# Optimization experiments

Hardware: AMD Instinct MI355X
Metric: run time of the kernel (lower is better)

The kernel has to match this reference:

```python
import jax, jax.numpy as jnp
import numpy as np

NUM_HEADS = 32
ROPE_BASE = 10000.0
MASK_NEG = -66504.0  # from (1 - tril) * -66504.0 in the source


def _rotate_half(x):
    d = x.shape[-1] // 2
    return jnp.concatenate([-x[..., d:], x[..., :d]], axis=-1)


def setup_inputs() -> dict:
    key = jax.random.key(0)
    k1, k2, k3, k4 = jax.random.split(key, 4)
    S, B, E = 2048, 2, 2048
    return {
        "hidden_states": jax.random.normal(k1, (S, B, E), dtype=jnp.float32) * 0.02,
        "qkv_w": jax.random.normal(k2, (E, 3 * E), dtype=jnp.float32) * 0.02,
        "qkv_b": jax.random.normal(k3, (3 * E,), dtype=jnp.float32) * 0.02,
        "out_w": jax.random.normal(k4, (E, E), dtype=jnp.float32) * 0.02,
        "out_b": jnp.zeros((E,), dtype=jnp.float32),
    }


def reference(hidden_states, qkv_w, qkv_b, out_w, out_b):
    # seq-first prompt/prefill path of IPEXTransformerAtten
    S, B, E = hidden_states.shape
    H = NUM_HEADS
    D = E // H

    # fused QKV projection (mm_qkv_out)
    qkv = jnp.einsum('sbe,ef->sbf', hidden_states, qkv_w) + qkv_b  # [S,B,3E]
    q, k, v = jnp.split(qkv, 3, axis=-1)
    q = q.reshape(S, B, H, D)
    k = k.reshape(S, B, H, D)
    v = v.reshape(S, B, H, D)

    # rotary embedding (GPT-NeoX style, full head_dim)
    inv_freq = 1.0 / (ROPE_BASE ** (jnp.arange(0, D, 2, dtype=jnp.float32) / D))
    freqs = jnp.arange(S, dtype=jnp.float32)[:, None] * inv_freq  # [S, D/2]
    emb = jnp.concatenate([freqs, freqs], axis=-1)  # [S, D]
    cos = jnp.cos(emb)[:, None, None, :].astype(hidden_states.dtype)
    sin = jnp.sin(emb)[:, None, None, :].astype(hidden_states.dtype)
    q = q * cos + _rotate_half(q) * sin
    k = k * cos + _rotate_half(k) * sin

    # scaled dot-product attention with causal mask
    scale = 1.0 / jnp.sqrt(jnp.array(D, dtype=hidden_states.dtype))
    scores = jnp.einsum('sbhd,tbhd->bhst', q, k) * scale  # [B,H,S,S]
    causal = jnp.tril(jnp.ones((S, S), dtype=scores.dtype))
    scores = scores + (1.0 - causal) * MASK_NEG
    attn = jax.nn.softmax(scores, axis=-1)
    ctx = jnp.einsum('bhst,tbhd->sbhd', attn, v).reshape(S, B, E)

    # output projection
    return jnp.einsum('sbe,ef->sbf', ctx, out_w) + out_b
```

## Files before the change

### kernel.cpp

```cpp
#include <hip/hip_runtime.h>
#include <hip/hip_bf16.h>

#define S_LEN 2048
#define BATCH 2
#define EMB   2048
#define NH    32
#define HD    64
#define M_ROWS (S_LEN * BATCH)
#define QKV_N  (3 * EMB)

typedef short bf16x8 __attribute__((ext_vector_type(8)));
typedef float f32x4  __attribute__((ext_vector_type(4)));

__device__ __forceinline__ unsigned short f2bf(float f) {
  unsigned int u = __float_as_uint(f);
  u += 0x7fffu + ((u >> 16) & 1u);
  return (unsigned short)(u >> 16);
}
__device__ __forceinline__ float bf2f(unsigned short h) {
  return __uint_as_float(((unsigned int)h) << 16);
}
__device__ __forceinline__ void async_copy16(const void* g, void* lds) {
  __builtin_amdgcn_global_load_lds(
      (const __attribute__((address_space(1))) void*)g,
      (__attribute__((address_space(3))) void*)lds, 16, 0, 0);
}

#if __has_builtin(__builtin_amdgcn_exp2f)
#define EXP2F(x) __builtin_amdgcn_exp2f(x)
#else
#define EXP2F(x) __expf((x) * 0.6931471805599453f)
#endif


__global__ __launch_bounds__(256) void cast_to_bf16(
    const float* __restrict__ in, unsigned short* __restrict__ out, int n4) {
  int i = blockIdx.x * 256 + threadIdx.x;
  if (i >= n4) return;
  float4 v = reinterpret_cast<const float4*>(in)[i];
  ushort4 o;
  o.x = f2bf(v.x); o.y = f2bf(v.y); o.z = f2bf(v.z); o.w = f2bf(v.w);
  reinterpret_cast<ushort4*>(out)[i] = o;
}

__global__ __launch_bounds__(256) void transpose_cast(
    const float* __restrict__ in, unsigned short* __restrict__ out, int R, int C) {
  __shared__ float tile[32][33];
  const int bc = blockIdx.x * 32, br = blockIdx.y * 32;
  const int tx = threadIdx.x & 31, ty = threadIdx.x >> 5;
  #pragma unroll
  for (int rr = ty; rr < 32; rr += 8)
    tile[rr][tx] = in[(size_t)(br + rr) * C + bc + tx];
  __syncthreads();
  #pragma unroll
  for (int rr = ty; rr < 32; rr += 8)
    out[(size_t)(bc + rr) * R + br + tx] = f2bf(tile[tx][rr]);
}


__global__ __launch_bounds__(256) void gemm_qkv(
    const unsigned short* __restrict__ A,
    const unsigned short* __restrict__ Wt,
    const float* __restrict__ bias,
    unsigned short* __restrict__ Qo,
    unsigned short* __restrict__ Ko,
    unsigned short* __restrict__ Vo) {
  __shared__ __align__(16) unsigned short As[128 * 32];
  __shared__ __align__(16) unsigned short Bs[128 * 32];
  const int tid = threadIdx.x;
  const int n0 = blockIdx.x * 128;
  const int m0 = blockIdx.y * 128;
  const int wave = tid >> 6, lane = tid & 63;
  const int wm = (wave >> 1) * 64, wn = (wave & 1) * 64;
  const int lm = lane & 15, lq = lane >> 4;
  const int K = 2048;

  const int r0 = tid >> 2, kc0 = (tid & 3) * 8;
  const unsigned short* Ar0 = A  + (size_t)(m0 + r0) * K + kc0;
  const unsigned short* Ar1 = Ar0 + (size_t)64 * K;
  const unsigned short* Br0 = Wt + (size_t)(n0 + r0) * K + kc0;
  const unsigned short* Br1 = Br0 + (size_t)64 * K;
  unsigned short* As0 = As + tid * 8;
  unsigned short* As1 = As + (tid + 256) * 8;
  unsigned short* Bs0 = Bs + tid * 8;
  unsigned short* Bs1 = Bs + (tid + 256) * 8;

  f32x4 acc[4][4] = {};

  for (int k0 = 0; k0 < K; k0 += 32) {
    async_copy16(Ar0 + k0, As0);
    async_copy16(Ar1 + k0, As1);
    async_copy16(Br0 + k0, Bs0);
    async_copy16(Br1 + k0, Bs1);
    __syncthreads();
    bf16x8 a[4], b[4];
    #pragma unroll
    for (int i = 0; i < 4; i++)
      a[i] = *reinterpret_cast<const bf16x8*>(As + (wm + i*16 + lm) * 32 + lq*8);
    #pragma unroll
    for (int j = 0; j < 4; j++)
      b[j] = *reinterpret_cast<const bf16x8*>(Bs + (wn + j*16 + lm) * 32 + lq*8);
    #pragma unroll
    for (int i = 0; i < 4; i++)
      #pragma unroll
      for (int j = 0; j < 4; j++)
        acc[i][j] = __builtin_amdgcn_mfma_f32_16x16x32_bf16(a[i], b[j], acc[i][j], 0, 0, 0);
    __syncthreads();
  }

  const int which = n0 >> 11;
  unsigned short* dst = (which == 0) ? Qo : (which == 1) ? Ko : Vo;
  #pragma unroll
  for (int j = 0; j < 4; j++) {
    const int n = n0 + wn + j*16 + lm;
    const float bv = bias[n];
    const int e = n & (EMB - 1), h = e >> 6, d = e & 63;
    #pragma unroll
    for (int i = 0; i < 4; i++) {
      #pragma unroll
      for (int r = 0; r < 4; r++) {
        const int m = m0 + wm + i*16 + lq*4 + r;
        const int s = m >> 1, b = m & 1;
        dst[(((size_t)b * NH + h) * S_LEN + s) * HD + d] = f2bf(acc[i][j][r] + bv);
      }
    }
  }
}


__global__ __launch_bounds__(256) void rope_kernel(
    unsigned short* __restrict__ Q, unsigned short* __restrict__ K) {
  const int idx = blockIdx.x * 256 + threadIdx.x;
  const int d  = idx & 31;
  const int s  = (idx >> 5) & (S_LEN - 1);
  const int bh = idx >> 16;
  const float inv_freq = __expf(d * -0.28782313662425575f);
  const float ang = (float)s * inv_freq;
  float sn, cs;
  __sincosf(ang, &sn, &cs);
  const size_t base = ((size_t)bh * S_LEN + s) * HD + d;
  float q1 = bf2f(Q[base]), q2 = bf2f(Q[base + 32]);
  Q[base]      = f2bf(q1 * cs - q2 * sn);
  Q[base + 32] = f2bf(q2 * cs + q1 * sn);
  float k1 = bf2f(K[base]), k2 = bf2f(K[base + 32]);
  K[base]      = f2bf(k1 * cs - k2 * sn);
  K[base + 32] = f2bf(k2 * cs + k1 * sn);
}


__global__ __launch_bounds__(256) void transpose_v(
    const unsigned short* __restrict__ V, unsigned short* __restrict__ VT) {
  __shared__ unsigned short t[64][65];
  const int bh = blockIdx.y;
  const int s0 = blockIdx.x * 64;
  const int tx = threadIdx.x & 63, ty = threadIdx.x >> 6;
  const unsigned short* src = V + ((size_t)bh * S_LEN + s0) * HD;
  #pragma unroll
  for (int r = ty; r < 64; r += 4)
    t[r][tx] = src[(size_t)r * HD + tx];
  __syncthreads();
  unsigned short* dst = VT + (size_t)bh * HD * S_LEN + s0;
  #pragma unroll
  for (int r = ty; r < 64; r += 4)
    dst[(size_t)r * S_LEN + tx] = t[tx][r];
}


__device__ __forceinline__ void attn_qblock(
    const char* __restrict__ Qb8,
    const char* __restrict__ Kb8,
    const char* __restrict__ Vb8,
    unsigned short* __restrict__ ctx,
    char* __restrict__ KsB,
    char* __restrict__ VsB,
    unsigned short* __restrict__ Pw,
    int q0, int b, int h, int tid, int wave, int lm, int lq) {
  const float C = 0.18033688011112042f;
  const int r0 = q0 + wave * 32;
  const int nt = (q0 >> 6) + 2;
  const int srow_c = r0 + lq * 4;

  const int srw = tid >> 2, sc16 = (tid & 3) * 16;

  bf16x8 qf[2][2];
  #pragma unroll
  for (int i = 0; i < 2; i++)
    #pragma unroll
    for (int ks = 0; ks < 2; ks++)
      qf[i][ks] = *reinterpret_cast<const bf16x8*>(
          Qb8 + (size_t)(r0 + i*16 + lm) * 128 + ks*64 + lq*16);

  f32x4 O[2][4] = {};
  float l[2][4] = {};

  for (int t = 0; t < nt; t++) {
    const int t0 = t * 64;
    async_copy16(Kb8 + (size_t)(t0 + srw) * 128      + sc16, KsB        + tid*16);
    async_copy16(Kb8 + (size_t)(t0 + srw) * 128 + 64 + sc16, KsB + 4096 + tid*16);
    async_copy16(Vb8 + (size_t)srw * 4096 + t0*2      + sc16, VsB        + tid*16);
    async_copy16(Vb8 + (size_t)srw * 4096 + t0*2 + 64 + sc16, VsB + 4096 + tid*16);
    __syncthreads();

    if (t0 <= r0 + 31) {
      const bool clean = (t0 + 63 <= r0);
      const int jmax  = clean ? 4 : ((r0 == t0) ? 2 : 4);
      const int kslim = clean ? 2 : ((r0 == t0) ? 1 : 2);

      f32x4 sc[2][4] = {};
      #pragma unroll
      for (int ks = 0; ks < 2; ks++) {
        bf16x8 kf[4];
        #pragma unroll
        for (int j = 0; j < 4; j++)
          if (j < jmax)
            kf[j] = *reinterpret_cast<const bf16x8*>(
                KsB + ks*4096 + (j*16 + lm)*64 + lq*16);
        #pragma unroll
        for (int i = 0; i < 2; i++)
          #pragma unroll
          for (int j = 0; j < 4; j++)
            if (j < jmax)
              sc[i][j] = __builtin_amdgcn_mfma_f32_16x16x32_bf16(qf[i][ks], kf[j], sc[i][j], 0, 0, 0);
      }

      if (clean) {
        #pragma unroll
        for (int i = 0; i < 2; i++)
          #pragma unroll
          for (int j = 0; j < 4; j++)
            #pragma unroll
            for (int r = 0; r < 4; r++) {
              const float p = EXP2F(sc[i][j][r] * C);
              l[i][r] += p;
              Pw[(i*16 + lq*4 + r) * 72 + j*16 + lm] = f2bf(p);
            }
      } else {
        #pragma unroll
        for (int i = 0; i < 2; i++)
          #pragma unroll
          for (int j = 0; j < 4; j++)
            if (j < jmax)
              #pragma unroll
              for (int r = 0; r < 4; r++) {
                const int srow = srow_c + i*16 + r;
                const int tcol = t0 + j*16 + lm;
                const float p = (tcol <= srow) ? EXP2F(sc[i][j][r] * C) : 0.0f;
                l[i][r] += p;
                Pw[(i*16 + lq*4 + r) * 72 + j*16 + lm] = f2bf(p);
              }
      }

      #pragma unroll
      for (int ks = 0; ks < 2; ks++) {
        if (ks < kslim) {
          bf16x8 pf[2], vf[4];
          #pragma unroll
          for (int i = 0; i < 2; i++)
            pf[i] = *reinterpret_cast<const bf16x8*>(Pw + (i*16 + lm)*72 + ks*32 + lq*8);
          #pragma unroll
          for (int j = 0; j < 4; j++)
            vf[j] = *reinterpret_cast<const bf16x8*>(
                VsB + ks*4096 + (j*16 + lm)*64 + lq*16);
          #pragma unroll
          for (int i = 0; i < 2; i++)
            #pragma unroll
            for (int j = 0; j < 4; j++)
              O[i][j] = __builtin_amdgcn_mfma_f32_16x16x32_bf16(pf[i], vf[j], O[i][j], 0, 0, 0);
        }
      }
    }
    __syncthreads();
  }

  #pragma unroll
  for (int i = 0; i < 2; i++) {
    #pragma unroll
    for (int r = 0; r < 4; r++) {
      float s = l[i][r];
      s += __shfl_xor(s, 1, 64);
      s += __shfl_xor(s, 2, 64);
      s += __shfl_xor(s, 4, 64);
      s += __shfl_xor(s, 8, 64);
      const float inv = 1.0f / s;
      const int srow = srow_c + i*16 + r;
      #pragma unroll
      for (int j = 0; j < 4; j++) {
        const int d = j*16 + lm;
        ctx[((size_t)srow * BATCH + b) * EMB + h*HD + d] = f2bf(O[i][j][r] * inv);
      }
    }
  }
}

__global__ __launch_bounds__(256) void attn_kernel(
    const unsigned short* __restrict__ Q,
    const unsigned short* __restrict__ K,
    const unsigned short* __restrict__ VT,
    unsigned short* __restrict__ ctx) {
  const int bh = blockIdx.x;
  const int p  = blockIdx.y;
  const int tid = threadIdx.x;
  const int wave = tid >> 6, lane = tid & 63;
  const int lm = lane & 15, lq = lane >> 4;
  const int b = bh >> 5, h = bh & 31;
  const char* Qb8 = (const char*)(Q  + (size_t)bh * S_LEN * HD);
  const char* Kb8 = (const char*)(K  + (size_t)bh * S_LEN * HD);
  const char* Vb8 = (const char*)(VT + (size_t)bh * HD * S_LEN);

  __shared__ __align__(16) unsigned short Ks[2][64][32];
  __shared__ __align__(16) unsigned short Vs[2][64][32];
  __shared__ __align__(16) unsigned short Pbuf[4][32][72];
  char* KsB = (char*)&Ks[0][0][0];
  char* VsB = (char*)&Vs[0][0][0];
  unsigned short* Pw = &Pbuf[wave][0][0];

  attn_qblock(Qb8, Kb8, Vb8, ctx, KsB, VsB, Pw, p * 128,        b, h, tid, wave, lm, lq);
  attn_qblock(Qb8, Kb8, Vb8, ctx, KsB, VsB, Pw, (15 - p) * 128, b, h, tid, wave, lm, lq);
}


__global__ __launch_bounds__(256) void gemm_out(
    const unsigned short* __restrict__ A,
    const unsigned short* __restrict__ Wt,
    const float* __restrict__ bias,
    float* __restrict__ out) {
  __shared__ __align__(16) unsigned short As[128 * 32];
  __shared__ __align__(16) unsigned short Bs[128 * 32];
  const int tid = threadIdx.x;
  const int n0 = blockIdx.x * 128;
  const int m0 = blockIdx.y * 128;
  const int wave = tid >> 6, lane = tid & 63;
  const int wm = (wave >> 1) * 64, wn = (wave & 1) * 64;
  const int lm = lane & 15, lq = lane >> 4;
  const int K = 2048;

  const int r0 = tid >> 2, kc0 = (tid & 3) * 8;
  const unsigned short* Ar0 = A  + (size_t)(m0 + r0) * K + kc0;
  const unsigned short* Ar1 = Ar0 + (size_t)64 * K;
  const unsigned short* Br0 = Wt + (size_t)(n0 + r0) * K + kc0;
  const unsigned short* Br1 = Br0 + (size_t)64 * K;
  unsigned short* As0 = As + tid * 8;
  unsigned short* As1 = As + (tid + 256) * 8;
  unsigned short* Bs0 = Bs + tid * 8;
  unsigned short* Bs1 = Bs + (tid + 256) * 8;

  f32x4 acc[4][4] = {};

  for (int k0 = 0; k0 < K; k0 += 32) {
    async_copy16(Ar0 + k0, As0);
    async_copy16(Ar1 + k0, As1);
    async_copy16(Br0 + k0, Bs0);
    async_copy16(Br1 + k0, Bs1);
    __syncthreads();
    bf16x8 a[4], b[4];
    #pragma unroll
    for (int i = 0; i < 4; i++)
      a[i] = *reinterpret_cast<const bf16x8*>(As + (wm + i*16 + lm) * 32 + lq*8);
    #pragma unroll
    for (int j = 0; j < 4; j++)
      b[j] = *reinterpret_cast<const bf16x8*>(Bs + (wn + j*16 + lm) * 32 + lq*8);
    #pragma unroll
    for (int i = 0; i < 4; i++)
      #pragma unroll
      for (int j = 0; j < 4; j++)
        acc[i][j] = __builtin_amdgcn_mfma_f32_16x16x32_bf16(a[i], b[j], acc[i][j], 0, 0, 0);
    __syncthreads();
  }

  #pragma unroll
  for (int j = 0; j < 4; j++) {
    const int n = n0 + wn + j*16 + lm;
    const float bv = bias[n];
    #pragma unroll
    for (int i = 0; i < 4; i++) {
      #pragma unroll
      for (int r = 0; r < 4; r++) {
        const int m = m0 + wm + i*16 + lq*4 + r;
        out[(size_t)m * EMB + n] = acc[i][j][r] + bv;
      }
    }
  }
}


extern "C" void kernel_launch(void* const* d_in, const int* in_sizes, int n_in,
                              void* d_out, int out_size, void* d_ws, size_t ws_size,
                              hipStream_t stream) {
  const float* hidden = (const float*)d_in[0];
  const float* qkv_w  = (const float*)d_in[1];
  const float* qkv_b  = (const float*)d_in[2];
  const float* out_w  = (const float*)d_in[3];
  const float* out_b  = (const float*)d_in[4];
  float* out = (float*)d_out;

  unsigned short* ws = (unsigned short*)d_ws;
  unsigned short* hbf   = ws;
  unsigned short* qkvwT = hbf   + (size_t)M_ROWS * EMB;
  unsigned short* outwT = qkvwT + (size_t)QKV_N * EMB;
  unsigned short* Qb    = outwT + (size_t)EMB * EMB;
  unsigned short* Kb    = Qb    + (size_t)64 * S_LEN * HD;
  unsigned short* Vb    = Kb    + (size_t)64 * S_LEN * HD;
  unsigned short* VTb   = Vb    + (size_t)64 * S_LEN * HD;
  unsigned short* ctx   = VTb   + (size_t)64 * S_LEN * HD;

  cast_to_bf16<<<(M_ROWS * EMB / 4) / 256, 256, 0, stream>>>(hidden, hbf, M_ROWS * EMB / 4);
  transpose_cast<<<dim3(QKV_N / 32, EMB / 32), 256, 0, stream>>>(qkv_w, qkvwT, EMB, QKV_N);
  transpose_cast<<<dim3(EMB / 32, EMB / 32), 256, 0, stream>>>(out_w, outwT, EMB, EMB);

  gemm_qkv<<<dim3(QKV_N / 128, M_ROWS / 128), 256, 0, stream>>>(hbf, qkvwT, qkv_b, Qb, Kb, Vb);

  rope_kernel<<<(64 * S_LEN * 32) / 256, 256, 0, stream>>>(Qb, Kb);
  transpose_v<<<dim3(S_LEN / 64, 64), 256, 0, stream>>>(Vb, VTb);

  attn_kernel<<<dim3(64, 8), 256, 0, stream>>>(Qb, Kb, VTb, ctx);

  gemm_out<<<dim3(EMB / 128, M_ROWS / 128), 256, 0, stream>>>(ctx, outwT, out_b, out);
}
```

Measured before the change: 423.8 us.

## Fuse RoPE into QKV GEMM epilogue and widen GEMM K-tile to 64

Applies the rotary embedding directly in the QKV projection epilogue, pairing accumulator columns d and d+32 within each wave, and removes the separate rope kernel with its extra read/write of Q and K. Both GEMMs now stage 64-wide K slices in a k-major LDS layout, halving the number of barrier-separated iterations. This doubles LDS per block and recomputes sincos per output element in the epilogue.

```diff
diff --git a/kernel.cpp b/kernel.cpp
--- a/kernel.cpp
+++ b/kernel.cpp
@@ -65,8 +65,8 @@
     unsigned short* __restrict__ Qo,
     unsigned short* __restrict__ Ko,
     unsigned short* __restrict__ Vo) {
-  __shared__ __align__(16) unsigned short As[128 * 32];
-  __shared__ __align__(16) unsigned short Bs[128 * 32];
+  __shared__ __align__(16) unsigned short As[128 * 64];
+  __shared__ __align__(16) unsigned short Bs[128 * 64];
   const int tid = threadIdx.x;
   const int n0 = blockIdx.x * 128;
   const int m0 = blockIdx.y * 128;
@@ -75,76 +75,84 @@
   const int lm = lane & 15, lq = lane >> 4;
   const int K = 2048;
 
-  const int r0 = tid >> 2, kc0 = (tid & 3) * 8;
-  const unsigned short* Ar0 = A  + (size_t)(m0 + r0) * K + kc0;
-  const unsigned short* Ar1 = Ar0 + (size_t)64 * K;
-  const unsigned short* Br0 = Wt + (size_t)(n0 + r0) * K + kc0;
-  const unsigned short* Br1 = Br0 + (size_t)64 * K;
-  unsigned short* As0 = As + tid * 8;
-  unsigned short* As1 = As + (tid + 256) * 8;
-  unsigned short* Bs0 = Bs + tid * 8;
-  unsigned short* Bs1 = Bs + (tid + 256) * 8;
+  const int srow = tid & 127;
+  const int sk0  = (tid >> 7) * 8;
+  const unsigned short* Ab = A  + (size_t)(m0 + srow) * K + sk0;
+  const unsigned short* Bb = Wt + (size_t)(n0 + srow) * K + sk0;
 
   f32x4 acc[4][4] = {};
 
-  for (int k0 = 0; k0 < K; k0 += 32) {
-    async_copy16(Ar0 + k0, As0);
-    async_copy16(Ar1 + k0, As1);
-    async_copy16(Br0 + k0, Bs0);
-    async_copy16(Br1 + k0, Bs1);
-    __syncthreads();
-    bf16x8 a[4], b[4];
-    #pragma unroll
-    for (int i = 0; i < 4; i++)
-      a[i] = *reinterpret_cast<const bf16x8*>(As + (wm + i*16 + lm) * 32 + lq*8);
-    #pragma unroll
-    for (int j = 0; j < 4; j++)
-      b[j] = *reinterpret_cast<const bf16x8*>(Bs + (wn + j*16 + lm) * 32 + lq*8);
-    #pragma unroll
-    for (int i = 0; i < 4; i++)
+  for (int k0 = 0; k0 < K; k0 += 64) {
+    #pragma unroll
+    for (int rep = 0; rep < 4; rep++) {
+      async_copy16(Ab + k0 + rep * 16, As + (size_t)(tid + 256 * rep) * 8);
+      async_copy16(Bb + k0 + rep * 16, Bs + (size_t)(tid + 256 * rep) * 8);
+    }
+    __syncthreads();
+    #pragma unroll
+    for (int ks = 0; ks < 2; ks++) {
+      bf16x8 a[4], b[4];
+      #pragma unroll
+      for (int i = 0; i < 4; i++)
+        a[i] = *reinterpret_cast<const bf16x8*>(
+            As + (size_t)((ks*4 + lq) * 128 + wm + i*16 + lm) * 8);
       #pragma unroll
       for (int j = 0; j < 4; j++)
-        acc[i][j] = __builtin_amdgcn_mfma_f32_16x16x32_bf16(a[i], b[j], acc[i][j], 0, 0, 0);
+        b[j] = *reinterpret_cast<const bf16x8*>(
+            Bs + (size_t)((ks*4 + lq) * 128 + wn + j*16 + lm) * 8);
+      #pragma unroll
+      for (int i = 0; i < 4; i++)
+        #pragma unroll
+        for (int j = 0; j < 4; j++)
+          acc[i][j] = __builtin_amdgcn_mfma_f32_16x16x32_bf16(a[i], b[j], acc[i][j], 0, 0, 0);
+    }
     __syncthreads();
   }
 
   const int which = n0 >> 11;
   unsigned short* dst = (which == 0) ? Qo : (which == 1) ? Ko : Vo;
-  #pragma unroll
-  for (int j = 0; j < 4; j++) {
-    const int n = n0 + wn + j*16 + lm;
-    const float bv = bias[n];
-    const int e = n & (EMB - 1), h = e >> 6, d = e & 63;
-    #pragma unroll
-    for (int i = 0; i < 4; i++) {
-      #pragma unroll
-      for (int r = 0; r < 4; r++) {
-        const int m = m0 + wm + i*16 + lq*4 + r;
-        const int s = m >> 1, b = m & 1;
-        dst[(((size_t)b * NH + h) * S_LEN + s) * HD + d] = f2bf(acc[i][j][r] + bv);
-      }
-    }
-  }
-}
-
-
-__global__ __launch_bounds__(256) void rope_kernel(
-    unsigned short* __restrict__ Q, unsigned short* __restrict__ K) {
-  const int idx = blockIdx.x * 256 + threadIdx.x;
-  const int d  = idx & 31;
-  const int s  = (idx >> 5) & (S_LEN - 1);
-  const int bh = idx >> 16;
-  const float inv_freq = __expf(d * -0.28782313662425575f);
-  const float ang = (float)s * inv_freq;
-  float sn, cs;
-  __sincosf(ang, &sn, &cs);
-  const size_t base = ((size_t)bh * S_LEN + s) * HD + d;
-  float q1 = bf2f(Q[base]), q2 = bf2f(Q[base + 32]);
-  Q[base]      = f2bf(q1 * cs - q2 * sn);
-  Q[base + 32] = f2bf(q2 * cs + q1 * sn);
-  float k1 = bf2f(K[base]), k2 = bf2f(K[base + 32]);
-  K[base]      = f2bf(k1 * cs - k2 * sn);
-  K[base + 32] = f2bf(k2 * cs + k1 * sn);
+  float bv[4];
+  #pragma unroll
+  for (int j = 0; j < 4; j++) bv[j] = bias[n0 + wn + j*16 + lm];
+
+  if (which < 2) {
+    #pragma unroll
+    for (int j = 0; j < 2; j++) {
+      const int n = n0 + wn + j*16 + lm;
+      const int e = n & (EMB - 1), h = e >> 6, d = e & 63;
+      const float invf = EXP2F((float)d * -0.4152410118609203f);
+      #pragma unroll
+      for (int i = 0; i < 4; i++) {
+        #pragma unroll
+        for (int r = 0; r < 4; r++) {
+          const int m = m0 + wm + i*16 + lq*4 + r;
+          const int s = m >> 1, b = m & 1;
+          const float v1 = acc[i][j][r]   + bv[j];
+          const float v2 = acc[i][j+2][r] + bv[j+2];
+          float sn, cs;
+          __sincosf((float)s * invf, &sn, &cs);
+          const size_t base = (((size_t)b * NH + h) * S_LEN + s) * HD + d;
+          dst[base]      = f2bf(v1 * cs - v2 * sn);
+          dst[base + 32] = f2bf(v2 * cs + v1 * sn);
+        }
+      }
+    }
+  } else {
+    #pragma unroll
+    for (int j = 0; j < 4; j++) {
+      const int n = n0 + wn + j*16 + lm;
+      const int e = n & (EMB - 1), h = e >> 6, d = e & 63;
+      #pragma unroll
+      for (int i = 0; i < 4; i++) {
+        #pragma unroll
+        for (int r = 0; r < 4; r++) {
+          const int m = m0 + wm + i*16 + lq*4 + r;
+          const int s = m >> 1, b = m & 1;
+          dst[(((size_t)b * NH + h) * S_LEN + s) * HD + d] = f2bf(acc[i][j][r] + bv[j]);
+        }
+      }
+    }
+  }
 }
 
 
@@ -324,8 +332,8 @@
     const unsigned short* __restrict__ Wt,
     const float* __restrict__ bias,
     float* __restrict__ out) {
-  __shared__ __align__(16) unsigned short As[128 * 32];
-  __shared__ __align__(16) unsigned short Bs[128 * 32];
+  __shared__ __align__(16) unsigned short As[128 * 64];
+  __shared__ __align__(16) unsigned short Bs[128 * 64];
   const int tid = threadIdx.x;
   const int n0 = blockIdx.x * 128;
   const int m0 = blockIdx.y * 128;
@@ -334,36 +342,37 @@
   const int lm = lane & 15, lq = lane >> 4;
   const int K = 2048;
 
-  const int r0 = tid >> 2, kc0 = (tid & 3) * 8;
-  const unsigned short* Ar0 = A  + (size_t)(m0 + r0) * K + kc0;
-  const unsigned short* Ar1 = Ar0 + (size_t)64 * K;
-  const unsigned short* Br0 = Wt + (size_t)(n0 + r0) * K + kc0;
-  const unsigned short* Br1 = Br0 + (size_t)64 * K;
-  unsigned short* As0 = As + tid * 8;
-  unsigned short* As1 = As + (tid + 256) * 8;
-  unsigned short* Bs0 = Bs + tid * 8;
-  unsigned short* Bs1 = Bs + (tid + 256) * 8;
+  const int srow = tid & 127;
+  const int sk0  = (tid >> 7) * 8;
+  const unsigned short* Ab = A  + (size_t)(m0 + srow) * K + sk0;
+  const unsigned short* Bb = Wt + (size_t)(n0 + srow) * K + sk0;
 
   f32x4 acc[4][4] = {};
 
-  for (int k0 = 0; k0 < K; k0 += 32) {
-    async_copy16(Ar0 + k0, As0);
-    async_copy16(Ar1 + k0, As1);
-    async_copy16(Br0 + k0, Bs0);
-    async_copy16(Br1 + k0, Bs1);
-    __syncthreads();
-    bf16x8 a[4], b[4];
-    #pragma unroll
-    for (int i = 0; i < 4; i++)
-      a[i] = *reinterpret_cast<const bf16x8*>(As + (wm + i*16 + lm) * 32 + lq*8);
-    #pragma unroll
-    for (int j = 0; j < 4; j++)
-      b[j] = *reinterpret_cast<const bf16x8*>(Bs + (wn + j*16 + lm) * 32 + lq*8);
-    #pragma unroll
-    for (int i = 0; i < 4; i++)
+  for (int k0 = 0; k0 < K; k0 += 64) {
+    #pragma unroll
+    for (int rep = 0; rep < 4; rep++) {
+      async_copy16(Ab + k0 + rep * 16, As + (size_t)(tid + 256 * rep) * 8);
+      async_copy16(Bb + k0 + rep * 16, Bs + (size_t)(tid + 256 * rep) * 8);
+    }
+    __syncthreads();
+    #pragma unroll
+    for (int ks = 0; ks < 2; ks++) {
+      bf16x8 a[4], b[4];
+      #pragma unroll
+      for (int i = 0; i < 4; i++)
+        a[i] = *reinterpret_cast<const bf16x8*>(
+            As + (size_t)((ks*4 + lq) * 128 + wm + i*16 + lm) * 8);
       #pragma unroll
       for (int j = 0; j < 4; j++)
-        acc[i][j] = __builtin_amdgcn_mfma_f32_16x16x32_bf16(a[i], b[j], acc[i][j], 0, 0, 0);
+        b[j] = *reinterpret_cast<const bf16x8*>(
+            Bs + (size_t)((ks*4 + lq) * 128 + wn + j*16 + lm) * 8);
+      #pragma unroll
+      for (int i = 0; i < 4; i++)
+        #pragma unroll
+        for (int j = 0; j < 4; j++)
+          acc[i][j] = __builtin_amdgcn_mfma_f32_16x16x32_bf16(a[i], b[j], acc[i][j], 0, 0, 0);
+    }
     __syncthreads();
   }
 
@@ -409,7 +418,6 @@
 
   gemm_qkv<<<dim3(QKV_N / 128, M_ROWS / 128), 256, 0, stream>>>(hbf, qkvwT, qkv_b, Qb, Kb, Vb);
 
-  rope_kernel<<<(64 * S_LEN * 32) / 256, 256, 0, stream>>>(Qb, Kb);
   transpose_v<<<dim3(S_LEN / 64, 64), 256, 0, stream>>>(Vb, VTb);
 
   attn_kernel<<<dim3(64, 8), 256, 0, stream>>>(Qb, Kb, VTb, ctx);
```

After: 527.5 us. +24.4%, slower.
